# Performance work log

Hardware: AMD Instinct MI355X
Metric: run time of the kernel (lower is better)

Reference implementation:

```python
import jax, jax.numpy as jnp
import numpy as np

N = 262144   # nodes
H = 256      # hidden_dim
NH = 8       # num_heads
HD = H // NH # head_dim = 32
C = 100      # num_commits
L = 2        # transformer layers


def _layer_norm(x, g, b, eps=1e-5):
    mu = jnp.mean(x, axis=-1, keepdims=True)
    var = jnp.mean(jnp.square(x - mu), axis=-1, keepdims=True)
    return (x - mu) * jax.lax.rsqrt(var + eps) * g + b


def setup_inputs() -> dict:
    key = jax.random.key(0)
    ks = jax.random.split(key, 16)
    w = lambda k, shape: jax.random.normal(k, shape, jnp.float32) * 0.02
    inp = {
        "node_embeddings": jax.random.normal(ks[0], (N, H), jnp.float32),
        "commit_indices": jax.random.randint(ks[1], (N,), 0, C),
        "num_commits": C,
        "commit_queries": jax.random.normal(ks[2], (NH, HD), jnp.float32),
        "k_w": w(ks[3], (H, H)), "k_b": jnp.zeros(H, jnp.float32),
        "v_w": w(ks[4], (H, H)), "v_b": jnp.zeros(H, jnp.float32),
        "po_w": w(ks[5], (H, H)), "po_b": jnp.zeros(H, jnp.float32),
        "pn_g": jnp.ones(H, jnp.float32), "pn_b": jnp.zeros(H, jnp.float32),
        "t_in_w": w(ks[6], (L, 3 * H, H)), "t_in_b": jnp.zeros((L, 3 * H), jnp.float32),
        "t_out_w": w(ks[7], (L, H, H)), "t_out_b": jnp.zeros((L, H), jnp.float32),
        "t_ln1_g": jnp.ones((L, H), jnp.float32), "t_ln1_b": jnp.zeros((L, H), jnp.float32),
        "t_ff1_w": w(ks[8], (L, 4 * H, H)), "t_ff1_b": jnp.zeros((L, 4 * H), jnp.float32),
        "t_ff2_w": w(ks[9], (L, H, 4 * H)), "t_ff2_b": jnp.zeros((L, H), jnp.float32),
        "t_ln2_g": jnp.ones((L, H), jnp.float32), "t_ln2_b": jnp.zeros((L, H), jnp.float32),
        "r1_w": w(ks[10], (H // 2, H)), "r1_b": jnp.zeros(H // 2, jnp.float32),
        "r2_w": w(ks[11], (1, H // 2)), "r2_b": jnp.zeros(1, jnp.float32),
    }
    return inp


def reference(node_embeddings, commit_indices, num_commits, commit_queries,
              k_w, k_b, v_w, v_b, po_w, po_b, pn_g, pn_b,
              t_in_w, t_in_b, t_out_w, t_out_b, t_ln1_g, t_ln1_b,
              t_ff1_w, t_ff1_b, t_ff2_w, t_ff2_b, t_ln2_g, t_ln2_b,
              r1_w, r1_b, r2_w, r2_b):
    nh, hd = commit_queries.shape
    scale = hd ** -0.5
    n = node_embeddings.shape[0]
    seg = commit_indices

    # --- segmented multi-head attention pooling (replaces per-commit loop) ---
    K = (node_embeddings @ k_w.T + k_b).reshape(n, nh, hd)   # [N,H,D]
    V = (node_embeddings @ v_w.T + v_b).reshape(n, nh, hd)
    scores = jnp.einsum('hd,nhd->nh', commit_queries, K) * scale  # [N,H]
    m = jax.ops.segment_max(scores, seg, num_segments=num_commits)  # [C,H]
    m = jnp.where(jnp.isfinite(m), m, 0.0)                          # empty commits
    e = jnp.exp(scores - m[seg])                                    # [N,H]
    den = jax.ops.segment_sum(e, seg, num_segments=num_commits)     # [C,H]
    num = jax.ops.segment_sum(e[:, :, None] * V, seg, num_segments=num_commits)  # [C,H,D]
    pooled = num / jnp.where(den > 0, den, 1.0)[:, :, None]
    counts = jax.ops.segment_sum(jnp.ones((n,), node_embeddings.dtype), seg,
                                 num_segments=num_commits)
    emb = _layer_norm(pooled.reshape(num_commits, nh * hd) @ po_w.T + po_b, pn_g, pn_b)
    x = jnp.where((counts > 0)[:, None], emb, 0.0)                  # [C,hidden]

    # --- commit transformer (seq len = C, batch = 1, post-norm, gelu) ---
    for l in range(t_in_w.shape[0]):
        qkv = x @ t_in_w[l].T + t_in_b[l]
        q, k, v = jnp.split(qkv, 3, axis=-1)
        q = q.reshape(num_commits, nh, hd)
        k = k.reshape(num_commits, nh, hd)
        v = v.reshape(num_commits, nh, hd)
        a = jax.nn.softmax(jnp.einsum('nhd,mhd->hnm', q, k) * scale, axis=-1)
        o = jnp.einsum('hnm,mhd->nhd', a, v).reshape(num_commits, nh * hd)
        o = o @ t_out_w[l].T + t_out_b[l]
        x = _layer_norm(x + o, t_ln1_g[l], t_ln1_b[l])
        ff = jax.nn.gelu(x @ t_ff1_w[l].T + t_ff1_b[l], approximate=False)
        ff = ff @ t_ff2_w[l].T + t_ff2_b[l]
        x = _layer_norm(x + ff, t_ln2_g[l], t_ln2_b[l])

    # --- ranking head ---
    h = jax.nn.gelu(x @ r1_w.T + r1_b, approximate=False)
    return (h @ r2_w.T + r2_b).squeeze(-1)  # [C]
```

## Files before the change

### kernel.cpp

```cpp
#include <hip/hip_runtime.h>
#include <math.h>

#define NNODES 262144
#define HDIM   256
#define NHEADS 8
#define HEADD  32
#define NC     100
#define NLAYER 2
#define SPLIT  15
#define NBLK   (NNODES/256)

__device__ __forceinline__ float gelu_exact(float v) {
    return 0.5f * v * (1.0f + erff(v * 0.70710678118654752440f));
}

__device__ __forceinline__ float dot4(float4 a, float4 b) {
    return a.x*b.x + a.y*b.y + a.z*b.z + a.w*b.w;
}

__device__ __forceinline__ float blk_sum256(float v, float* red, int tid) {
    #pragma unroll
    for (int m = 32; m >= 1; m >>= 1) v += __shfl_xor(v, m, 64);
    if ((tid & 63) == 0) red[tid >> 6] = v;
    __syncthreads();
    float tot = red[0] + red[1] + red[2] + red[3];
    __syncthreads();
    return tot;
}

__global__ void k_qkw(const float* __restrict__ q, const float* __restrict__ kw,
                      const float* __restrict__ kb, float* __restrict__ qk_w,
                      float* __restrict__ qk_b) {
    int h = blockIdx.x, j = threadIdx.x;
    float s = 0.f;
    #pragma unroll
    for (int d = 0; d < HEADD; ++d) s += q[h*HEADD + d] * kw[(h*HEADD + d)*HDIM + j];
    qk_w[h*HDIM + j] = s;
    if (j == 0) {
        float sb = 0.f;
        #pragma unroll
        for (int d = 0; d < HEADD; ++d) sb += q[h*HEADD + d] * kb[h*HEADD + d];
        qk_b[h] = sb;
    }
}

__global__ __launch_bounds__(256, 6) void k_score(const float* __restrict__ emb,
        const float* __restrict__ qk_w, const float* __restrict__ qk_b,
        float* __restrict__ ev_out) {
    int tid = threadIdx.x, w = tid >> 6, lane = tid & 63;
    int s = lane & 7;
    int gw = blockIdx.x * 4 + w;
    int r0 = gw * 64;
    const float scale = 0.17677669529663688f;

    float4 w4[NHEADS];
    #pragma unroll
    for (int h = 0; h < NHEADS; ++h)
        w4[h] = ((const float4*)(qk_w + h*HDIM))[lane];
    float qkb_s = qk_b[s];

    const float4* base4 = (const float4*)(emb + (size_t)r0 * HDIM);
    float keep = 0.f;

    auto PROC = [&](float4 cur, int r) {
        float p[NHEADS];
        #pragma unroll
        for (int h = 0; h < NHEADS; ++h) p[h] = dot4(cur, w4[h]);
        float q0, q1, q2, q3;
        {
            bool sel = (s & 1) != 0;
            float a0 = __shfl_xor(p[0], 1, 64), a1 = __shfl_xor(p[1], 1, 64);
            q0 = sel ? (p[1] + a1) : (p[0] + a0);
            float a2 = __shfl_xor(p[2], 1, 64), a3 = __shfl_xor(p[3], 1, 64);
            q1 = sel ? (p[3] + a3) : (p[2] + a2);
            float a4 = __shfl_xor(p[4], 1, 64), a5 = __shfl_xor(p[5], 1, 64);
            q2 = sel ? (p[5] + a5) : (p[4] + a4);
            float a6 = __shfl_xor(p[6], 1, 64), a7 = __shfl_xor(p[7], 1, 64);
            q3 = sel ? (p[7] + a7) : (p[6] + a6);
        }
        float r0v, r1v;
        {
            bool sel = (s & 2) != 0;
            float b0 = __shfl_xor(q0, 2, 64), b1 = __shfl_xor(q1, 2, 64);
            r0v = sel ? (q1 + b1) : (q0 + b0);
            float b2 = __shfl_xor(q2, 2, 64), b3 = __shfl_xor(q3, 2, 64);
            r1v = sel ? (q3 + b3) : (q2 + b2);
        }
        float tt;
        {
            bool sel = (s & 4) != 0;
            float c0 = __shfl_xor(r0v, 4, 64), c1 = __shfl_xor(r1v, 4, 64);
            tt = sel ? (r1v + c1) : (r0v + c0);
        }
        tt += __shfl_xor(tt, 8, 64);
        tt += __shfl_xor(tt, 16, 64);
        tt += __shfl_xor(tt, 32, 64);
        float evv = __expf((tt + qkb_s) * scale);
        if ((lane >> 3) == (r & 7)) keep = evv;
        if ((r & 7) == 7)
            ev_out[(size_t)(r0 + r - 7) * NHEADS + lane] = keep;
    };

    float4 eA = base4[lane];
    #pragma unroll 4
    for (int r = 0; r < 64; r += 2) {
        float4 eB = base4[(r + 1) * 64 + lane];
        PROC(eA, r);
        if (r + 2 < 64) eA = base4[(r + 2) * 64 + lane];
        PROC(eB, r + 1);
    }
}

__global__ __launch_bounds__(256) void k_hist(const int* __restrict__ cidx,
                                              int* __restrict__ hist) {
    __shared__ int l_hist[NC];
    int tid = threadIdx.x;
    for (int i = tid; i < NC; i += 256) l_hist[i] = 0;
    __syncthreads();
    int c = cidx[blockIdx.x * 256 + tid];
    atomicAdd(&l_hist[c], 1);
    __syncthreads();
    for (int i = tid; i < NC; i += 256) hist[blockIdx.x*NC + i] = l_hist[i];
}

__global__ __launch_bounds__(256) void k_blockscan(const int* __restrict__ hist,
        int* __restrict__ bbase, int* __restrict__ counts) {
    int c = blockIdx.x, t = threadIdx.x;
    int v[4]; int loc = 0;
    #pragma unroll
    for (int i = 0; i < 4; ++i) { v[i] = hist[(t*4 + i)*NC + c]; loc += v[i]; }
    __shared__ int sc[256];
    sc[t] = loc; __syncthreads();
    for (int off = 1; off < 256; off <<= 1) {
        int x = (t >= off) ? sc[t - off] : 0;
        __syncthreads();
        sc[t] += x;
        __syncthreads();
    }
    int run = (t > 0) ? sc[t-1] : 0;
    #pragma unroll
    for (int i = 0; i < 4; ++i) { bbase[(t*4 + i)*NC + c] = run; run += v[i]; }
    if (t == 255) counts[c] = sc[255];
}

__global__ void k_scan(const int* __restrict__ counts, int* __restrict__ offs) {
    __shared__ int sc[128];
    int t = threadIdx.x;
    int v = (t < NC) ? counts[t] : 0;
    sc[t] = v; __syncthreads();
    for (int off = 1; off < 128; off <<= 1) {
        int x = (t >= off) ? sc[t - off] : 0;
        __syncthreads();
        sc[t] += x;
        __syncthreads();
    }
    if (t <= NC) offs[t] = sc[t] - v;
}

__global__ __launch_bounds__(256) void k_scatter(const int* __restrict__ cidx,
        const int* __restrict__ offs, const int* __restrict__ bbase,
        int* __restrict__ nlist) {
    __shared__ int sb[NC];
    __shared__ int lcur[NC];
    int t = threadIdx.x, blk = blockIdx.x;
    if (t < NC) { sb[t] = offs[t] + bbase[blk*NC + t]; lcur[t] = 0; }
    __syncthreads();
    int n = blk * 256 + t;
    int c = cidx[n];
    int p = atomicAdd(&lcur[c], 1);
    nlist[sb[c] + p] = n;
}

__global__ __launch_bounds__(256, 6) void k_accum(const float* __restrict__ emb,
        const float* __restrict__ ev, const int* __restrict__ nlist,
        const int* __restrict__ offs, const int* __restrict__ counts,
        float* __restrict__ S_part, float* __restrict__ den_part) {
    int c  = blockIdx.x / SPLIT;
    int sl = blockIdx.x % SPLIT;
    int cnt = counts[c];
    __shared__ float s_buf[2][NHEADS*HDIM];
    __shared__ float s_den[2][NHEADS];
    int tid = threadIdx.x, w = tid >> 6, lane = tid & 63;
    int i = lane >> 3;

    float4 acc[NHEADS];
    #pragma unroll
    for (int h = 0; h < NHEADS; ++h) acc[h] = make_float4(0.f, 0.f, 0.f, 0.f);
    float4 den_a = make_float4(0.f, 0.f, 0.f, 0.f);
    float4 den_b = make_float4(0.f, 0.f, 0.f, 0.f);

    int beg = offs[c];
    int per = (cnt + SPLIT - 1) / SPLIT;
    int s0 = min(cnt, sl * per), s1 = min(cnt, s0 + per);

#define ROWLOAD(nreg, e_, va_, vb_)                                          \
    e_  = ((const float4*)(emb + (size_t)(nreg) * HDIM))[lane];              \
    va_ = *(const float4*)(ev + (size_t)(nreg) * NHEADS);                    \
    vb_ = *(const float4*)(ev + (size_t)(nreg) * NHEADS + 4);

    int base = s0 + w*8;
    int nn = 0;
    if (base < s1) {
        int nb0 = min(8, s1 - base);
        if (i < nb0) nn = nlist[beg + base + i];
    }
    for (; base < s1; base += 32) {
        int nb = min(8, s1 - base);
        int nn_next = 0;
        int base2 = base + 32;
        if (base2 < s1) {
            int nb2 = min(8, s1 - base2);
            if (i < nb2) nn_next = nlist[beg + base2 + i];
        }
        float4 eA, eB, vaA, vbA, vaB, vbB;
        int n0 = __shfl(nn, 0, 64);
        ROWLOAD(n0, eA, vaA, vbA);
        #pragma unroll
        for (int i2 = 0; i2 < 8; ++i2) {
            if (i2 >= nb) break;
            if (i2 + 1 < nb) {
                int nx = __shfl(nn, (i2 + 1) * 8, 64);
                if ((i2 & 1) == 0) { ROWLOAD(nx, eB, vaB, vbB); }
                else               { ROWLOAD(nx, eA, vaA, vbA); }
            }
            float4 e_c  = (i2 & 1) ? eB  : eA;
            float4 va_c = (i2 & 1) ? vaB : vaA;
            float4 vb_c = (i2 & 1) ? vbB : vbA;
            den_a.x += va_c.x; den_a.y += va_c.y; den_a.z += va_c.z; den_a.w += va_c.w;
            den_b.x += vb_c.x; den_b.y += vb_c.y; den_b.z += vb_c.z; den_b.w += vb_c.w;
            acc[0].x += va_c.x * e_c.x; acc[0].y += va_c.x * e_c.y;
            acc[0].z += va_c.x * e_c.z; acc[0].w += va_c.x * e_c.w;
            acc[1].x += va_c.y * e_c.x; acc[1].y += va_c.y * e_c.y;
            acc[1].z += va_c.y * e_c.z; acc[1].w += va_c.y * e_c.w;
            acc[2].x += va_c.z * e_c.x; acc[2].y += va_c.z * e_c.y;
            acc[2].z += va_c.z * e_c.z; acc[2].w += va_c.z * e_c.w;
            acc[3].x += va_c.w * e_c.x; acc[3].y += va_c.w * e_c.y;
            acc[3].z += va_c.w * e_c.z; acc[3].w += va_c.w * e_c.w;
            acc[4].x += vb_c.x * e_c.x; acc[4].y += vb_c.x * e_c.y;
            acc[4].z += vb_c.x * e_c.z; acc[4].w += vb_c.x * e_c.w;
            acc[5].x += vb_c.y * e_c.x; acc[5].y += vb_c.y * e_c.y;
            acc[5].z += vb_c.y * e_c.z; acc[5].w += vb_c.y * e_c.w;
            acc[6].x += vb_c.z * e_c.x; acc[6].y += vb_c.z * e_c.y;
            acc[6].z += vb_c.z * e_c.z; acc[6].w += vb_c.z * e_c.w;
            acc[7].x += vb_c.w * e_c.x; acc[7].y += vb_c.w * e_c.y;
            acc[7].z += vb_c.w * e_c.z; acc[7].w += vb_c.w * e_c.w;
        }
        nn = nn_next;
    }
#undef ROWLOAD

    if (w >= 2) {
        #pragma unroll
        for (int h2 = 0; h2 < NHEADS; ++h2)
            ((float4*)&s_buf[w-2][h2*HDIM])[lane] = acc[h2];
        if (lane == 0) {
            s_den[w-2][0] = den_a.x; s_den[w-2][1] = den_a.y;
            s_den[w-2][2] = den_a.z; s_den[w-2][3] = den_a.w;
            s_den[w-2][4] = den_b.x; s_den[w-2][5] = den_b.y;
            s_den[w-2][6] = den_b.z; s_den[w-2][7] = den_b.w;
        }
    }
    __syncthreads();
    if (w < 2) {
        #pragma unroll
        for (int h2 = 0; h2 < NHEADS; ++h2) {
            float4 v = ((const float4*)&s_buf[w][h2*HDIM])[lane];
            acc[h2].x += v.x; acc[h2].y += v.y; acc[h2].z += v.z; acc[h2].w += v.w;
        }
        den_a.x += s_den[w][0]; den_a.y += s_den[w][1];
        den_a.z += s_den[w][2]; den_a.w += s_den[w][3];
        den_b.x += s_den[w][4]; den_b.y += s_den[w][5];
        den_b.z += s_den[w][6]; den_b.w += s_den[w][7];
    }
    __syncthreads();
    if (w == 1) {
        #pragma unroll
        for (int h2 = 0; h2 < NHEADS; ++h2)
            ((float4*)&s_buf[0][h2*HDIM])[lane] = acc[h2];
        if (lane == 0) {
            s_den[0][0] = den_a.x; s_den[0][1] = den_a.y;
            s_den[0][2] = den_a.z; s_den[0][3] = den_a.w;
            s_den[0][4] = den_b.x; s_den[0][5] = den_b.y;
            s_den[0][6] = den_b.z; s_den[0][7] = den_b.w;
        }
    }
    __syncthreads();
    if (w == 0) {
        float* Sd = S_part + ((size_t)sl*NC + c) * (NHEADS*HDIM);
        #pragma unroll
        for (int h2 = 0; h2 < NHEADS; ++h2) {
            float4 v = ((const float4*)&s_buf[0][h2*HDIM])[lane];
            v.x += acc[h2].x; v.y += acc[h2].y; v.z += acc[h2].z; v.w += acc[h2].w;
            ((float4*)(Sd + h2*HDIM))[lane] = v;
        }
        if (lane == 0) {
            float* dp = den_part + ((size_t)sl*NC + c) * NHEADS;
            dp[0] = den_a.x + s_den[0][0]; dp[1] = den_a.y + s_den[0][1];
            dp[2] = den_a.z + s_den[0][2]; dp[3] = den_a.w + s_den[0][3];
            dp[4] = den_b.x + s_den[0][4]; dp[5] = den_b.y + s_den[0][5];
            dp[6] = den_b.z + s_den[0][6]; dp[7] = den_b.w + s_den[0][7];
        }
    }
}

__global__ __launch_bounds__(256) void k_pool(const float* __restrict__ S_part,
        const float* __restrict__ den_part, const int* __restrict__ counts,
        const float* __restrict__ vw, const float* __restrict__ vb,
        const float* __restrict__ pow_, const float* __restrict__ pob,
        const float* __restrict__ png, const float* __restrict__ pnb,
        float* __restrict__ x) {
    int c = blockIdx.x, t = threadIdx.x;
    __shared__ float S_l[NHEADS*HDIM];
    __shared__ float pooled[HDIM];
    __shared__ float red[4];
    {
        float4 a0 = make_float4(0.f,0.f,0.f,0.f), a1 = a0;
        #pragma unroll
        for (int sl = 0; sl < SPLIT; ++sl) {
            const float4* sp = (const float4*)(S_part + ((size_t)sl*NC + c) * (NHEADS*HDIM));
            float4 v0 = sp[t], v1 = sp[t + 256];
            a0.x += v0.x; a0.y += v0.y; a0.z += v0.z; a0.w += v0.w;
            a1.x += v1.x; a1.y += v1.y; a1.z += v1.z; a1.w += v1.w;
        }
        ((float4*)S_l)[t] = a0;
        ((float4*)S_l)[t + 256] = a1;
    }
    int h = t >> 5;
    float dh = 0.f;
    #pragma unroll
    for (int sl = 0; sl < SPLIT; ++sl) dh += den_part[(sl*NC + c)*NHEADS + h];
    __syncthreads();
    float dx = dh > 0.f ? dh : 1.f;
    float s = vb[t] * dh;
    const float4* wr = (const float4*)(vw + (size_t)t * HDIM);
    const float4* sr = (const float4*)(S_l + h * HDIM);
    #pragma unroll 8
    for (int j = 0; j < HDIM/4; ++j) s += dot4(wr[j], sr[j]);
    pooled[t] = s / dx;
    __syncthreads();
    float o = pob[t];
    const float4* pr = (const float4*)(pow_ + (size_t)t * HDIM);
    const float4* pv = (const float4*)pooled;
    #pragma unroll 8
    for (int j = 0; j < HDIM/4; ++j) o += dot4(pr[j], pv[j]);
    float mu  = blk_sum256(o, red, t) * (1.f/256.f);
    float d   = o - mu;
    float var = blk_sum256(d*d, red, t) * (1.f/256.f);
    float y = d * rsqrtf(var + 1e-5f) * png[t] + pnb[t];
    x[c*HDIM + t] = (counts[c] > 0) ? y : 0.f;
}

__global__ __launch_bounds__(256) void k_mm(const float* __restrict__ in,
        const float* __restrict__ W, const float* __restrict__ bias,
        float* __restrict__ out, int K, int P, int do_gelu) {
    int r = blockIdx.x;
    int p = blockIdx.y * 256 + threadIdx.x;
    __shared__ float xr[1024];
    for (int idx = threadIdx.x; idx < K; idx += 256) xr[idx] = in[(size_t)r*K + idx];
    __syncthreads();
    float s = bias[p];
    const float4* wr = (const float4*)(W + (size_t)p * K);
    const float4* xv = (const float4*)xr;
    for (int j = 0; j < (K >> 2); ++j) s += dot4(wr[j], xv[j]);
    if (do_gelu) s = gelu_exact(s);
    out[(size_t)r*P + p] = s;
}

__global__ __launch_bounds__(256) void k_mm_res_ln(const float* __restrict__ in,
        const float* __restrict__ W, const float* __restrict__ bias,
        const float* __restrict__ g, const float* __restrict__ be,
        float* __restrict__ x, int K) {
    int r = blockIdx.x, t = threadIdx.x;
    __shared__ float xr[1024];
    __shared__ float red[4];
    for (int idx = t; idx < K; idx += 256) xr[idx] = in[(size_t)r*K + idx];
    __syncthreads();
    float s = bias[t];
    const float4* wr = (const float4*)(W + (size_t)t * K);
    const float4* xv = (const float4*)xr;
    for (int j = 0; j < (K >> 2); ++j) s += dot4(wr[j], xv[j]);
    float v = x[r*HDIM + t] + s;
    float mu  = blk_sum256(v, red, t) * (1.f/256.f);
    float d   = v - mu;
    float var = blk_sum256(d*d, red, t) * (1.f/256.f);
    x[r*HDIM + t] = d * rsqrtf(var + 1e-5f) * g[t] + be[t];
}

__global__ __launch_bounds__(256) void k_attn(const float* __restrict__ qkv,
        float* __restrict__ attn_out) {
    int h = blockIdx.x, t = threadIdx.x;
    __shared__ float k_l[NC * HEADD];
    __shared__ float sc[NC * NC];
    for (int idx = t; idx < NC*HEADD; idx += 256) {
        int n = idx >> 5, d = idx & 31;
        k_l[idx] = qkv[n*768 + 256 + h*HEADD + d];
    }
    __syncthreads();
    const float scale = 0.17677669529663688f;
    for (int idx = t; idx < NC*NC; idx += 256) {
        int n = idx / NC, m = idx - n*NC;
        const float4* q4 = (const float4*)(qkv + n*768 + h*HEADD);
        const float4* k4 = (const float4*)(k_l + m*HEADD);
        float s = 0.f;
        #pragma unroll
        for (int j = 0; j < HEADD/4; ++j) s += dot4(q4[j], k4[j]);
        sc[idx] = s * scale;
    }
    __syncthreads();
    if (t < NC) {
        float mx = -1e30f;
        for (int m = 0; m < NC; ++m) mx = fmaxf(mx, sc[t*NC + m]);
        float sum = 0.f;
        for (int m = 0; m < NC; ++m) { float e = expf(sc[t*NC + m] - mx); sc[t*NC + m] = e; sum += e; }
        float inv = 1.f / sum;
        for (int m = 0; m < NC; ++m) sc[t*NC + m] *= inv;
    }
    __syncthreads();
    for (int idx = t; idx < NC*HEADD; idx += 256) {
        int n = idx >> 5, d = idx & 31;
        float o = 0.f;
        for (int m = 0; m < NC; ++m) o += sc[n*NC + m] * qkv[m*768 + 512 + h*HEADD + d];
        attn_out[n*HDIM + h*HEADD + d] = o;
    }
}

__global__ __launch_bounds__(128) void k_head(const float* __restrict__ x,
        const float* __restrict__ r1w, const float* __restrict__ r1b,
        const float* __restrict__ r2w, const float* __restrict__ r2b,
        float* __restrict__ out) {
    int r = blockIdx.x, t = threadIdx.x;
    __shared__ float xr[HDIM];
    __shared__ float red[2];
    xr[t] = x[r*HDIM + t];
    xr[t + 128] = x[r*HDIM + t + 128];
    __syncthreads();
    float s = r1b[t];
    const float4* wr = (const float4*)(r1w + (size_t)t * HDIM);
    const float4* xv = (const float4*)xr;
    #pragma unroll 8
    for (int j = 0; j < HDIM/4; ++j) s += dot4(wr[j], xv[j]);
    s = gelu_exact(s);
    float contrib = s * r2w[t];
    #pragma unroll
    for (int m = 32; m >= 1; m >>= 1) contrib += __shfl_xor(contrib, m, 64);
    if ((t & 63) == 0) red[t >> 6] = contrib;
    __syncthreads();
    if (t == 0) out[r] = red[0] + red[1] + r2b[0];
}

extern "C" void kernel_launch(void* const* d_in, const int* in_sizes, int n_in,
                              void* d_out, int out_size, void* d_ws, size_t ws_size,
                              hipStream_t stream) {
    const float* emb   = (const float*)d_in[0];
    const int*   cidx  = (const int*)d_in[1];
    const float* q     = (const float*)d_in[3];
    const float* kw    = (const float*)d_in[4];
    const float* kb    = (const float*)d_in[5];
    const float* vw    = (const float*)d_in[6];
    const float* vb    = (const float*)d_in[7];
    const float* pow_  = (const float*)d_in[8];
    const float* pob   = (const float*)d_in[9];
    const float* png   = (const float*)d_in[10];
    const float* pnb   = (const float*)d_in[11];
    const float* tinw  = (const float*)d_in[12];
    const float* tinb  = (const float*)d_in[13];
    const float* toutw = (const float*)d_in[14];
    const float* toutb = (const float*)d_in[15];
    const float* ln1g  = (const float*)d_in[16];
    const float* ln1b  = (const float*)d_in[17];
    const float* ff1w  = (const float*)d_in[18];
    const float* ff1b  = (const float*)d_in[19];
    const float* ff2w  = (const float*)d_in[20];
    const float* ff2b  = (const float*)d_in[21];
    const float* ln2g  = (const float*)d_in[22];
    const float* ln2b  = (const float*)d_in[23];
    const float* r1w   = (const float*)d_in[24];
    const float* r1b   = (const float*)d_in[25];
    const float* r2w   = (const float*)d_in[26];
    const float* r2b   = (const float*)d_in[27];
    float* out = (float*)d_out;

    char* ws = (char*)d_ws;
    size_t off = 0;
    auto alloc = [&](size_t bytes) -> char* {
        off = (off + 255) & ~(size_t)255;
        char* p = ws + off;
        off += bytes;
        return p;
    };
    int*   hist   = (int*)alloc((size_t)NBLK * NC * 4);
    int*   bbase  = (int*)alloc((size_t)NBLK * NC * 4);
    int*   counts = (int*)alloc(NC * 4);
    int*   offs   = (int*)alloc((NC + 1) * 4);
    float* den_p  = (float*)alloc((size_t)SPLIT * NC * NHEADS * 4);
    float* S_part = (float*)alloc((size_t)SPLIT * NC * NHEADS * HDIM * 4);
    float* qk_w   = (float*)alloc(NHEADS * HDIM * 4);
    float* qk_b   = (float*)alloc(NHEADS * 4);
    int*   nlist  = (int*)alloc((size_t)NNODES * 4);
    float* x      = (float*)alloc(NC * HDIM * 4);
    float* qkv    = (float*)alloc(NC * 3 * HDIM * 4);
    float* attn_o = (float*)alloc(NC * HDIM * 4);
    float* ffb    = (float*)alloc(NC * 4 * HDIM * 4);
    float* ev     = (float*)alloc((size_t)NNODES * NHEADS * 4);
    (void)ws_size; (void)in_sizes; (void)n_in; (void)out_size;

    k_qkw<<<NHEADS, HDIM, 0, stream>>>(q, kw, kb, qk_w, qk_b);
    k_score<<<NBLK, 256, 0, stream>>>(emb, qk_w, qk_b, ev);
    k_hist<<<NBLK, 256, 0, stream>>>(cidx, hist);
    k_blockscan<<<NC, 256, 0, stream>>>(hist, bbase, counts);
    k_scan<<<1, 128, 0, stream>>>(counts, offs);
    k_scatter<<<NBLK, 256, 0, stream>>>(cidx, offs, bbase, nlist);
    k_accum<<<NC*SPLIT, 256, 0, stream>>>(emb, ev, nlist, offs, counts, S_part, den_p);
    k_pool<<<NC, 256, 0, stream>>>(S_part, den_p, counts, vw, vb, pow_, pob, png, pnb, x);

    for (int l = 0; l < NLAYER; ++l) {
        k_mm<<<dim3(NC, 3), 256, 0, stream>>>(x, tinw + (size_t)l*3*HDIM*HDIM,
                                              tinb + (size_t)l*3*HDIM, qkv, HDIM, 3*HDIM, 0);
        k_attn<<<NHEADS, 256, 0, stream>>>(qkv, attn_o);
        k_mm_res_ln<<<NC, 256, 0, stream>>>(attn_o, toutw + (size_t)l*HDIM*HDIM,
                                            toutb + (size_t)l*HDIM, ln1g + (size_t)l*HDIM,
                                            ln1b + (size_t)l*HDIM, x, HDIM);
        k_mm<<<dim3(NC, 4), 256, 0, stream>>>(x, ff1w + (size_t)l*4*HDIM*HDIM,
                                              ff1b + (size_t)l*4*HDIM, ffb, HDIM, 4*HDIM, 1);
        k_mm_res_ln<<<NC, 256, 0, stream>>>(ffb, ff2w + (size_t)l*HDIM*4*HDIM,
                                            ff2b + (size_t)l*HDIM, ln2g + (size_t)l*HDIM,
                                            ln2b + (size_t)l*HDIM, x, 4*HDIM);
    }
    k_head<<<NC, 128, 0, stream>>>(x, r1w, r1b, r2w, r2b, out);
}
```

Before: 772.0 us.

## Fuse attention score computation into gathered accumulation kernel, drop separate score pass

```diff
diff --git a/kernel.cpp b/kernel.cpp
--- a/kernel.cpp
+++ b/kernel.cpp
@@ -7,7 +7,7 @@
 #define HEADD  32
 #define NC     100
 #define NLAYER 2
-#define SPLIT  15
+#define SPLIT  10
 #define NBLK   (NNODES/256)
 
 __device__ __forceinline__ float gelu_exact(float v) {
@@ -41,73 +41,6 @@
         #pragma unroll
         for (int d = 0; d < HEADD; ++d) sb += q[h*HEADD + d] * kb[h*HEADD + d];
         qk_b[h] = sb;
-    }
-}
-
-__global__ __launch_bounds__(256, 6) void k_score(const float* __restrict__ emb,
-        const float* __restrict__ qk_w, const float* __restrict__ qk_b,
-        float* __restrict__ ev_out) {
-    int tid = threadIdx.x, w = tid >> 6, lane = tid & 63;
-    int s = lane & 7;
-    int gw = blockIdx.x * 4 + w;
-    int r0 = gw * 64;
-    const float scale = 0.17677669529663688f;
-
-    float4 w4[NHEADS];
-    #pragma unroll
-    for (int h = 0; h < NHEADS; ++h)
-        w4[h] = ((const float4*)(qk_w + h*HDIM))[lane];
-    float qkb_s = qk_b[s];
-
-    const float4* base4 = (const float4*)(emb + (size_t)r0 * HDIM);
-    float keep = 0.f;
-
-    auto PROC = [&](float4 cur, int r) {
-        float p[NHEADS];
-        #pragma unroll
-        for (int h = 0; h < NHEADS; ++h) p[h] = dot4(cur, w4[h]);
-        float q0, q1, q2, q3;
-        {
-            bool sel = (s & 1) != 0;
-            float a0 = __shfl_xor(p[0], 1, 64), a1 = __shfl_xor(p[1], 1, 64);
-            q0 = sel ? (p[1] + a1) : (p[0] + a0);
-            float a2 = __shfl_xor(p[2], 1, 64), a3 = __shfl_xor(p[3], 1, 64);
-            q1 = sel ? (p[3] + a3) : (p[2] + a2);
-            float a4 = __shfl_xor(p[4], 1, 64), a5 = __shfl_xor(p[5], 1, 64);
-            q2 = sel ? (p[5] + a5) : (p[4] + a4);
-            float a6 = __shfl_xor(p[6], 1, 64), a7 = __shfl_xor(p[7], 1, 64);
-            q3 = sel ? (p[7] + a7) : (p[6] + a6);
-        }
-        float r0v, r1v;
-        {
-            bool sel = (s & 2) != 0;
-            float b0 = __shfl_xor(q0, 2, 64), b1 = __shfl_xor(q1, 2, 64);
-            r0v = sel ? (q1 + b1) : (q0 + b0);
-            float b2 = __shfl_xor(q2, 2, 64), b3 = __shfl_xor(q3, 2, 64);
-            r1v = sel ? (q3 + b3) : (q2 + b2);
-        }
-        float tt;
-        {
-            bool sel = (s & 4) != 0;
-            float c0 = __shfl_xor(r0v, 4, 64), c1 = __shfl_xor(r1v, 4, 64);
-            tt = sel ? (r1v + c1) : (r0v + c0);
-        }
-        tt += __shfl_xor(tt, 8, 64);
-        tt += __shfl_xor(tt, 16, 64);
-        tt += __shfl_xor(tt, 32, 64);
-        float evv = __expf((tt + qkb_s) * scale);
-        if ((lane >> 3) == (r & 7)) keep = evv;
-        if ((r & 7) == 7)
-            ev_out[(size_t)(r0 + r - 7) * NHEADS + lane] = keep;
-    };
-
-    float4 eA = base4[lane];
-    #pragma unroll 4
-    for (int r = 0; r < 64; r += 2) {
-        float4 eB = base4[(r + 1) * 64 + lane];
-        PROC(eA, r);
-        if (r + 2 < 64) eA = base4[(r + 2) * 64 + lane];
-        PROC(eB, r + 1);
     }
 }
 
@@ -171,17 +104,25 @@
     nlist[sb[c] + p] = n;
 }
 
-__global__ __launch_bounds__(256, 6) void k_accum(const float* __restrict__ emb,
-        const float* __restrict__ ev, const int* __restrict__ nlist,
-        const int* __restrict__ offs, const int* __restrict__ counts,
-        float* __restrict__ S_part, float* __restrict__ den_part) {
+__global__ __launch_bounds__(256, 4) void k_accum(const float* __restrict__ emb,
+        const int* __restrict__ nlist, const int* __restrict__ offs,
+        const int* __restrict__ counts, const float* __restrict__ qk_w,
+        const float* __restrict__ qk_b, float* __restrict__ S_part,
+        float* __restrict__ den_part) {
     int c  = blockIdx.x / SPLIT;
     int sl = blockIdx.x % SPLIT;
     int cnt = counts[c];
     __shared__ float s_buf[2][NHEADS*HDIM];
     __shared__ float s_den[2][NHEADS];
     int tid = threadIdx.x, w = tid >> 6, lane = tid & 63;
-    int i = lane >> 3;
+    int s = lane & 7, i = lane >> 3;
+    const float scale = 0.17677669529663688f;
+
+    float4 w4[NHEADS];
+    #pragma unroll
+    for (int h = 0; h < NHEADS; ++h)
+        w4[h] = ((const float4*)(qk_w + h*HDIM))[lane];
+    float qkb_s = qk_b[s];
 
     float4 acc[NHEADS];
     #pragma unroll
@@ -193,10 +134,9 @@
     int per = (cnt + SPLIT - 1) / SPLIT;
     int s0 = min(cnt, sl * per), s1 = min(cnt, s0 + per);
 
-#define ROWLOAD(nreg, e_, va_, vb_)                                          \
-    e_  = ((const float4*)(emb + (size_t)(nreg) * HDIM))[lane];              \
-    va_ = *(const float4*)(ev + (size_t)(nreg) * NHEADS);                    \
-    vb_ = *(const float4*)(ev + (size_t)(nreg) * NHEADS + 4);
+#define ISSUE(j_, buf_) {                                                    \
+    int nx_ = __shfl(nn, (j_)*8, 64);                                        \
+    buf_ = ((const float4*)(emb + (size_t)nx_ * HDIM))[lane]; }
 
     int base = s0 + w*8;
     int nn = 0;
@@ -212,42 +152,79 @@
             int nb2 = min(8, s1 - base2);
             if (i < nb2) nn_next = nlist[beg + base2 + i];
         }
-        float4 eA, eB, vaA, vbA, vaB, vbB;
-        int n0 = __shfl(nn, 0, 64);
-        ROWLOAD(n0, eA, vaA, vbA);
+        float4 e0, e1, e2, e3;
+        ISSUE(0, e0);
+        if (1 < nb) ISSUE(1, e1);
+        if (2 < nb) ISSUE(2, e2);
+        if (3 < nb) ISSUE(3, e3);
         #pragma unroll
         for (int i2 = 0; i2 < 8; ++i2) {
             if (i2 >= nb) break;
-            if (i2 + 1 < nb) {
-                int nx = __shfl(nn, (i2 + 1) * 8, 64);
-                if ((i2 & 1) == 0) { ROWLOAD(nx, eB, vaB, vbB); }
-                else               { ROWLOAD(nx, eA, vaA, vbA); }
+            float4 e_c;
+            if      ((i2 & 3) == 0) { e_c = e0; if (i2 + 4 < nb) ISSUE(i2 + 4, e0) }
+            else if ((i2 & 3) == 1) { e_c = e1; if (i2 + 4 < nb) ISSUE(i2 + 4, e1) }
+            else if ((i2 & 3) == 2) { e_c = e2; if (i2 + 4 < nb) ISSUE(i2 + 4, e2) }
+            else                    { e_c = e3; if (i2 + 4 < nb) ISSUE(i2 + 4, e3) }
+            float p[NHEADS];
+            #pragma unroll
+            for (int h = 0; h < NHEADS; ++h) p[h] = dot4(e_c, w4[h]);
+            float q0, q1, q2, q3;
+            {
+                bool sel = (s & 1) != 0;
+                float a0 = __shfl_xor(p[0], 1, 64), a1 = __shfl_xor(p[1], 1, 64);
+                q0 = sel ? (p[1] + a1) : (p[0] + a0);
+                float a2 = __shfl_xor(p[2], 1, 64), a3 = __shfl_xor(p[3], 1, 64);
+                q1 = sel ? (p[3] + a3) : (p[2] + a2);
+                float a4 = __shfl_xor(p[4], 1, 64), a5 = __shfl_xor(p[5], 1, 64);
+                q2 = sel ? (p[5] + a5) : (p[4] + a4);
+                float a6 = __shfl_xor(p[6], 1, 64), a7 = __shfl_xor(p[7], 1, 64);
+                q3 = sel ? (p[7] + a7) : (p[6] + a6);
             }
-            float4 e_c  = (i2 & 1) ? eB  : eA;
-            float4 va_c = (i2 & 1) ? vaB : vaA;
-            float4 vb_c = (i2 & 1) ? vbB : vbA;
-            den_a.x += va_c.x; den_a.y += va_c.y; den_a.z += va_c.z; den_a.w += va_c.w;
-            den_b.x += vb_c.x; den_b.y += vb_c.y; den_b.z += vb_c.z; den_b.w += vb_c.w;
-            acc[0].x += va_c.x * e_c.x; acc[0].y += va_c.x * e_c.y;
-            acc[0].z += va_c.x * e_c.z; acc[0].w += va_c.x * e_c.w;
-            acc[1].x += va_c.y * e_c.x; acc[1].y += va_c.y * e_c.y;
-            acc[1].z += va_c.y * e_c.z; acc[1].w += va_c.y * e_c.w;
-            acc[2].x += va_c.z * e_c.x; acc[2].y += va_c.z * e_c.y;
-            acc[2].z += va_c.z * e_c.z; acc[2].w += va_c.z * e_c.w;
-            acc[3].x += va_c.w * e_c.x; acc[3].y += va_c.w * e_c.y;
-            acc[3].z += va_c.w * e_c.z; acc[3].w += va_c.w * e_c.w;
-            acc[4].x += vb_c.x * e_c.x; acc[4].y += vb_c.x * e_c.y;
-            acc[4].z += vb_c.x * e_c.z; acc[4].w += vb_c.x * e_c.w;
-            acc[5].x += vb_c.y * e_c.x; acc[5].y += vb_c.y * e_c.y;
-            acc[5].z += vb_c.y * e_c.z; acc[5].w += vb_c.y * e_c.w;
-            acc[6].x += vb_c.z * e_c.x; acc[6].y += vb_c.z * e_c.y;
-            acc[6].z += vb_c.z * e_c.z; acc[6].w += vb_c.z * e_c.w;
-            acc[7].x += vb_c.w * e_c.x; acc[7].y += vb_c.w * e_c.y;
-            acc[7].z += vb_c.w * e_c.z; acc[7].w += vb_c.w * e_c.w;
+            float r0v, r1v;
+            {
+                bool sel = (s & 2) != 0;
+                float b0 = __shfl_xor(q0, 2, 64), b1 = __shfl_xor(q1, 2, 64);
+                r0v = sel ? (q1 + b1) : (q0 + b0);
+                float b2 = __shfl_xor(q2, 2, 64), b3 = __shfl_xor(q3, 2, 64);
+                r1v = sel ? (q3 + b3) : (q2 + b2);
+            }
+            float tt;
+            {
+                bool sel = (s & 4) != 0;
+                float c0 = __shfl_xor(r0v, 4, 64), c1 = __shfl_xor(r1v, 4, 64);
+                tt = sel ? (r1v + c1) : (r0v + c0);
+            }
+            tt += __shfl_xor(tt, 8, 64);
+            tt += __shfl_xor(tt, 16, 64);
+            tt += __shfl_xor(tt, 32, 64);
+            float evv = __expf((tt + qkb_s) * scale);
+            float4 va, vb;
+            va.x = __shfl(evv, 0, 8); va.y = __shfl(evv, 1, 8);
+            va.z = __shfl(evv, 2, 8); va.w = __shfl(evv, 3, 8);
+            vb.x = __shfl(evv, 4, 8); vb.y = __shfl(evv, 5, 8);
+            vb.z = __shfl(evv, 6, 8); vb.w = __shfl(evv, 7, 8);
+            den_a.x += va.x; den_a.y += va.y; den_a.z += va.z; den_a.w += va.w;
+            den_b.x += vb.x; den_b.y += vb.y; den_b.z += vb.z; den_b.w += vb.w;
+            acc[0].x += va.x * e_c.x; acc[0].y += va.x * e_c.y;
+            acc[0].z += va.x * e_c.z; acc[0].w += va.x * e_c.w;
+            acc[1].x += va.y * e_c.x; acc[1].y += va.y * e_c.y;
+            acc[1].z += va.y * e_c.z; acc[1].w += va.y * e_c.w;
+            acc[2].x += va.z * e_c.x; acc[2].y += va.z * e_c.y;
+            acc[2].z += va.z * e_c.z; acc[2].w += va.z * e_c.w;
+            acc[3].x += va.w * e_c.x; acc[3].y += va.w * e_c.y;
+            acc[3].z += va.w * e_c.z; acc[3].w += va.w * e_c.w;
+            acc[4].x += vb.x * e_c.x; acc[4].y += vb.x * e_c.y;
+            acc[4].z += vb.x * e_c.z; acc[4].w += vb.x * e_c.w;
+            acc[5].x += vb.y * e_c.x; acc[5].y += vb.y * e_c.y;
+            acc[5].z += vb.y * e_c.z; acc[5].w += vb.y * e_c.w;
+            acc[6].x += vb.z * e_c.x; acc[6].y += vb.z * e_c.y;
+            acc[6].z += vb.z * e_c.z; acc[6].w += vb.z * e_c.w;
+            acc[7].x += vb.w * e_c.x; acc[7].y += vb.w * e_c.y;
+            acc[7].z += vb.w * e_c.z; acc[7].w += vb.w * e_c.w;
         }
         nn = nn_next;
     }
-#undef ROWLOAD
+#undef ISSUE
 
     if (w >= 2) {
         #pragma unroll
@@ -501,16 +478,14 @@
     float* qkv    = (float*)alloc(NC * 3 * HDIM * 4);
     float* attn_o = (float*)alloc(NC * HDIM * 4);
     float* ffb    = (float*)alloc(NC * 4 * HDIM * 4);
-    float* ev     = (float*)alloc((size_t)NNODES * NHEADS * 4);
     (void)ws_size; (void)in_sizes; (void)n_in; (void)out_size;
 
     k_qkw<<<NHEADS, HDIM, 0, stream>>>(q, kw, kb, qk_w, qk_b);
-    k_score<<<NBLK, 256, 0, stream>>>(emb, qk_w, qk_b, ev);
     k_hist<<<NBLK, 256, 0, stream>>>(cidx, hist);
     k_blockscan<<<NC, 256, 0, stream>>>(hist, bbase, counts);
     k_scan<<<1, 128, 0, stream>>>(counts, offs);
     k_scatter<<<NBLK, 256, 0, stream>>>(cidx, offs, bbase, nlist);
-    k_accum<<<NC*SPLIT, 256, 0, stream>>>(emb, ev, nlist, offs, counts, S_part, den_p);
+    k_accum<<<NC*SPLIT, 256, 0, stream>>>(emb, nlist, offs, counts, qk_w, qk_b, S_part, den_p);
     k_pool<<<NC, 256, 0, stream>>>(S_part, den_p, counts, vw, vb, pow_, pob, png, pnb, x);
 
     for (int l = 0; l < NLAYER; ++l) {
```

Result: faster. 741.9 us (-3.9%).
